# Performance work log

Hardware: AMD Instinct MI355X
Metric: run time of the kernel (lower is better)

## Reference

```python
import jax, jax.numpy as jnp
import numpy as np


def setup_inputs() -> dict:
    key = jax.random.key(0)
    kq, kk, kv = jax.random.split(key, 3)
    B, L, S, H, E = 4, 2048, 2048, 16, 64
    queries = jax.random.normal(kq, (B, L, H, E), dtype=jnp.float32)
    keys = jax.random.normal(kk, (B, S, H, E), dtype=jnp.float32)
    values = jax.random.normal(kv, (B, S, H, E), dtype=jnp.float32)
    return {"queries": queries, "keys": keys, "values": values}


def reference(queries, keys, values):
    # queries: [b,l,h,e], keys: [b,s,h,e], values: [b,s,h,d]
    e = queries.shape[-1]
    scale = 1.0 / jnp.sqrt(jnp.asarray(e, dtype=queries.dtype))
    scores = jnp.einsum('blhe,bshe->bhls', queries, keys)  # [b,h,l,s]
    attn_map = jax.nn.softmax(scale * scores, axis=-1)
    # dropout is identity in eval/reference mode
    v = jnp.einsum('bhls,bshd->blhd', attn_map, values)  # [b,l,h,d]
    return v, attn_map
```

## Files before the change

### kernel.cpp

```cpp
#include <hip/hip_runtime.h>
#include <hip/hip_bf16.h>


typedef __attribute__((ext_vector_type(4)))  float  f32x4;
typedef __attribute__((ext_vector_type(8)))  short  short8;
typedef __attribute__((ext_vector_type(4)))  short  short4v;
typedef __attribute__((ext_vector_type(4)))  unsigned short u16x4;

__device__ __forceinline__ unsigned short bf(float x) {
  return __builtin_bit_cast(unsigned short, __float2bfloat16(x));
}

__device__ __forceinline__ float bf2f(unsigned short u) {
  return __builtin_bit_cast(float, (unsigned int)u << 16);
}

__device__ __forceinline__ unsigned short f2bf(float f) {
  unsigned int u = __builtin_bit_cast(unsigned int, f);
  return (unsigned short)((u + 0x7FFFu + ((u >> 16) & 1u)) >> 16);
}

#define MFMA16(A, Bv, C) __builtin_amdgcn_mfma_f32_16x16x32_bf16(A, Bv, C, 0, 0, 0)


__global__ __launch_bounds__(256) void conv_all(const float* __restrict__ K,
                                                const float* __restrict__ V,
                                                unsigned short* __restrict__ Kbf,
                                                unsigned short* __restrict__ VTbf) {
  __shared__ unsigned short T[64][68];
  if (blockIdx.x < 4096) {
    int idx = blockIdx.x * 256 + threadIdx.x;
    int e0 = (idx & 7) << 3;
    int h  = (idx >> 3) & 15;
    int l  = (idx >> 7) & 2047;
    int b  = idx >> 18;
    const float* src = K + (((size_t)(b * 2048 + l)) * 16 + h) * 64 + e0;
    unsigned short* dst = Kbf + (((size_t)(b * 16 + h)) * 2048 + l) * 64 + e0;
    float4 a = *(const float4*)src;
    float4 c = *(const float4*)(src + 4);
    u16x4 o0 = { bf(a.x), bf(a.y), bf(a.z), bf(a.w) };
    u16x4 o1 = { bf(c.x), bf(c.y), bf(c.z), bf(c.w) };
    *(u16x4*)dst = o0;
    *(u16x4*)(dst + 4) = o1;
  } else {
    int bid = blockIdx.x - 4096;
    int sc = bid & 31, bh = bid >> 5;
    int h = bh & 15, b = bh >> 4;
    int t = threadIdx.x;
    int srow = t >> 2, d0 = (t & 3) << 4;
    const float* src = V + (((size_t)(b * 2048 + sc * 64 + srow)) * 16 + h) * 64 + d0;
    float4 v0 = *(const float4*)(src + 0);
    float4 v1 = *(const float4*)(src + 4);
    float4 v2 = *(const float4*)(src + 8);
    float4 v3 = *(const float4*)(src + 12);
    T[d0+ 0][srow]=bf(v0.x); T[d0+ 1][srow]=bf(v0.y); T[d0+ 2][srow]=bf(v0.z); T[d0+ 3][srow]=bf(v0.w);
    T[d0+ 4][srow]=bf(v1.x); T[d0+ 5][srow]=bf(v1.y); T[d0+ 6][srow]=bf(v1.z); T[d0+ 7][srow]=bf(v1.w);
    T[d0+ 8][srow]=bf(v2.x); T[d0+ 9][srow]=bf(v2.y); T[d0+10][srow]=bf(v2.z); T[d0+11][srow]=bf(v2.w);
    T[d0+12][srow]=bf(v3.x); T[d0+13][srow]=bf(v3.y); T[d0+14][srow]=bf(v3.z); T[d0+15][srow]=bf(v3.w);
    __syncthreads();
    int d = t >> 2, s0 = (t & 3) << 4;
    unsigned short* dst = VTbf + ((size_t)bh * 64 + d) * 2048 + sc * 64 + s0;
#pragma unroll
    for (int j = 0; j < 16; j += 4) {
      u16x4 x = { T[d][s0 + j], T[d][s0 + j + 1], T[d][s0 + j + 2], T[d][s0 + j + 3] };
      *(u16x4*)(dst + j) = x;
    }
  }
}


__device__ __forceinline__ void gll16(const void* g, void* l) {
  __builtin_amdgcn_global_load_lds(
      (const __attribute__((address_space(1))) unsigned int*)g,
      (__attribute__((address_space(3))) unsigned int*)l, 16, 0, 0);
}

__device__ __forceinline__ void stage8(const unsigned short* gsrc, int rowStride,
                                       unsigned short* dstRow0, int lane) {
  int rr = lane >> 3;
  int cc = ((lane & 7) ^ rr) << 3;
  gll16(gsrc + (size_t)rr * rowStride + cc, dstRow0);
}

__device__ __forceinline__ short8 frag(const unsigned short* tile, int row, int colb) {
  return *(const short8*)((const char*)tile + row * 128 + (colb ^ ((row & 7) << 4)));
}

__global__ __launch_bounds__(512, 2) void attn_main(
    const float* __restrict__ Qf, const unsigned short* __restrict__ Kbf,
    const unsigned short* __restrict__ VTbf, float* __restrict__ Og,
    float* __restrict__ Ag) {

  int wg = ((blockIdx.x & 7) << 7) | (blockIdx.x >> 3);
  int qt = wg & 15, bh = wg >> 4;
  int h = bh & 15, b = bh >> 4;

  int tid = threadIdx.x, lane = tid & 63, w = tid >> 6;
  int g = lane >> 4, r16 = lane & 15;
  int q0 = qt * 128;

  __shared__ __align__(16) unsigned short Qb[128][64];
  __shared__ __align__(16) unsigned short Kb[2][64][64];
  __shared__ __align__(16) unsigned short Vb[2][64][64];
  __shared__ __align__(16) unsigned short Pb[8][16][72];

  const unsigned short* kg = Kbf + (size_t)bh * 2048 * 64 + (size_t)(w * 8) * 64;
  const unsigned short* vg = VTbf + (size_t)bh * 64 * 2048 + (size_t)(w * 8) * 2048;

  {
    const float sc = 0.18033688011112042f;
    int row = tid >> 2, c0 = (tid & 3) << 4;
    const float* qsrc = Qf + (((size_t)(b * 2048 + q0 + row)) * 16 + h) * 64 + c0;
    float4 qa = *(const float4*)(qsrc + 0);
    float4 qb = *(const float4*)(qsrc + 4);
    float4 qc = *(const float4*)(qsrc + 8);
    float4 qd = *(const float4*)(qsrc + 12);
    stage8(kg,            64, &Kb[0][w * 8][0], lane);
    stage8(kg + 4096,     64, &Kb[1][w * 8][0], lane);
    stage8(kg + 2 * 4096, 64, &Vb[0][w * 8][0], lane);
    stage8(kg + 3 * 4096, 64, &Vb[1][w * 8][0], lane);
    unsigned short* qdst = &Qb[row][c0];
    u16x4 o0 = { bf(qa.x*sc), bf(qa.y*sc), bf(qa.z*sc), bf(qa.w*sc) };
    u16x4 o1 = { bf(qb.x*sc), bf(qb.y*sc), bf(qb.z*sc), bf(qb.w*sc) };
    u16x4 o2 = { bf(qc.x*sc), bf(qc.y*sc), bf(qc.z*sc), bf(qc.w*sc) };
    u16x4 o3 = { bf(qd.x*sc), bf(qd.y*sc), bf(qd.z*sc), bf(qd.w*sc) };
    *(u16x4*)(qdst + 0) = o0;  *(u16x4*)(qdst + 4)  = o1;
    *(u16x4*)(qdst + 8) = o2;  *(u16x4*)(qdst + 12) = o3;
  }
  asm volatile("s_waitcnt lgkmcnt(0)" ::: "memory");
  __builtin_amdgcn_s_barrier();

  short8 qf0 = *(const short8*)((const char*)&Qb[w * 16 + r16][0] + g * 16);
  short8 qf1 = *(const short8*)((const char*)&Qb[w * 16 + r16][0] + 64 + g * 16);

  float lsum = 0.0f;
  for (int ii = 0; ii < 16; ++ii) {
    const int hsel = ii & 1;
    const unsigned short* sA = hsel ? &Vb[0][0][0] : &Kb[0][0][0];
    const unsigned short* sB = hsel ? &Vb[1][0][0] : &Kb[1][0][0];

    if (ii < 15) {
      asm volatile("s_waitcnt vmcnt(2)" ::: "memory");
    } else {
      asm volatile("s_waitcnt vmcnt(0)" ::: "memory");
    }
    __builtin_amdgcn_s_barrier();

    f32x4 st[8];
    __builtin_amdgcn_s_setprio(1);
#pragma unroll
    for (int t = 0; t < 4; ++t) {
      short8 kf0 = frag(sA, t * 16 + r16, g * 16);
      short8 kf1 = frag(sA, t * 16 + r16, 64 + g * 16);
      f32x4 z = {0.f, 0.f, 0.f, 0.f};
      z = MFMA16(kf0, qf0, z);
      z = MFMA16(kf1, qf1, z);
      st[t] = z;
    }
#pragma unroll
    for (int t = 0; t < 4; ++t) {
      short8 kf0 = frag(sB, t * 16 + r16, g * 16);
      short8 kf1 = frag(sB, t * 16 + r16, 64 + g * 16);
      f32x4 z = {0.f, 0.f, 0.f, 0.f};
      z = MFMA16(kf0, qf0, z);
      z = MFMA16(kf1, qf1, z);
      st[t + 4] = z;
    }
    __builtin_amdgcn_s_setprio(0);

    float acc = 0.f;
#pragma unroll
    for (int t = 0; t < 8; ++t) {
      float e0 = __builtin_amdgcn_exp2f(st[t][0]) + __builtin_amdgcn_exp2f(st[t][1]);
      float e1 = __builtin_amdgcn_exp2f(st[t][2]) + __builtin_amdgcn_exp2f(st[t][3]);
      acc += e0 + e1;
    }
    lsum += acc;

    __builtin_amdgcn_s_barrier();

    if (ii < 14) {
      const unsigned short* nk = kg + (size_t)(2 * ii + 4) * 4096;
      unsigned short* dA = hsel ? &Vb[0][w * 8][0] : &Kb[0][w * 8][0];
      unsigned short* dB = hsel ? &Vb[1][w * 8][0] : &Kb[1][w * 8][0];
      stage8(nk,        64, dA, lane);
      stage8(nk + 4096, 64, dB, lane);
    }
  }
  lsum += __shfl_xor(lsum, 16, 64);
  lsum += __shfl_xor(lsum, 32, 64);
  float rinv = 1.0f / lsum;

  f32x4 oacc[4];
#pragma unroll
  for (int t = 0; t < 4; ++t) oacc[t] = (f32x4){0.f, 0.f, 0.f, 0.f};

  stage8(kg, 64, &Kb[0][w * 8][0], lane);
  stage8(vg, 2048, &Vb[0][w * 8][0], lane);
  asm volatile("s_waitcnt vmcnt(0)" ::: "memory");
  __builtin_amdgcn_s_barrier();
  int cur = 0;

  float* aW = Ag + ((size_t)bh * 2048 + (size_t)(q0 + w * 16)) * 2048;
  const int sra = lane >> 4;
  const int src4 = (lane & 15) * 4;

  for (int ch = 0; ch < 32; ++ch) {
    if (ch < 31) {
      stage8(kg + (size_t)(ch + 1) * 4096, 64, &Kb[cur ^ 1][w * 8][0], lane);
      stage8(vg + (size_t)(ch + 1) * 64, 2048, &Vb[cur ^ 1][w * 8][0], lane);
    }
    f32x4 st[4];
    __builtin_amdgcn_s_setprio(1);
#pragma unroll
    for (int t = 0; t < 4; ++t) {
      short8 kf0 = frag(&Kb[cur][0][0], t * 16 + r16, g * 16);
      short8 kf1 = frag(&Kb[cur][0][0], t * 16 + r16, 64 + g * 16);
      f32x4 z = {0.f, 0.f, 0.f, 0.f};
      z = MFMA16(kf0, qf0, z);
      z = MFMA16(kf1, qf1, z);
      st[t] = z;
    }
    __builtin_amdgcn_s_setprio(0);

#pragma unroll
    for (int t = 0; t < 4; ++t) {
      f32x4 p;
#pragma unroll
      for (int r = 0; r < 4; ++r)
        p[r] = __builtin_amdgcn_exp2f(st[t][r]) * rinv;
      u16x4 pb = { bf(p[0]), bf(p[1]), bf(p[2]), bf(p[3]) };
      *(u16x4*)&Pb[w][r16][t * 16 + 4 * g] = pb;
    }

#pragma unroll
    for (int i = 0; i < 4; ++i) {
      int row = 4 * i + sra;
      u16x4 pb4 = *(const u16x4*)&Pb[w][row][src4];
      f32x4 o = { bf2f(pb4[0]), bf2f(pb4[1]), bf2f(pb4[2]), bf2f(pb4[3]) };
      __builtin_nontemporal_store(o, (f32x4*)(aW + (size_t)row * 2048 + ch * 64 + src4));
    }

    __builtin_amdgcn_s_setprio(1);
#pragma unroll
    for (int c = 0; c < 2; ++c) {
      short8 pa = *(const short8*)((const char*)&Pb[w][r16][0] + c * 64 + g * 16);
#pragma unroll
      for (int t = 0; t < 4; ++t) {
        short8 vf = frag(&Vb[cur][0][0], t * 16 + r16, c * 64 + g * 16);
        oacc[t] = MFMA16(pa, vf, oacc[t]);
      }
    }
    __builtin_amdgcn_s_setprio(0);

    asm volatile("s_waitcnt vmcnt(4)" ::: "memory");
    __builtin_amdgcn_s_barrier();
    cur ^= 1;
  }

  float* op = Og + (((size_t)b * 2048 + (size_t)(q0 + w * 16 + 4 * g)) * 16 + h) * 64;
#pragma unroll
  for (int t = 0; t < 4; ++t)
#pragma unroll
    for (int r = 0; r < 4; ++r)
      op[(size_t)r * 1024 + t * 16 + r16] = oacc[t][r];
}


__global__ __launch_bounds__(256, 2) void attn_fused(
    const float* __restrict__ Qg, const float* __restrict__ Kg,
    const float* __restrict__ Vg, float* __restrict__ Og,
    float* __restrict__ Ag) {

  const int qt = blockIdx.x & 31;
  const int bh = blockIdx.x >> 5;
  const int h  = bh & 15;
  const int b  = bh >> 4;

  const int tid  = threadIdx.x;
  const int lane = tid & 63;
  const int w    = tid >> 6;
  const int g    = lane >> 4;
  const int r16  = lane & 15;

  __shared__ __align__(16) unsigned short Qbuf[64][72];
  __shared__ __align__(16) unsigned short Kbuf[64][72];
  __shared__ __align__(16) unsigned short VT[64][68];
  __shared__ __align__(16) unsigned short Pbuf[4][16][72];

  const size_t inbase = (size_t)b * (2048u * 1024u) + (size_t)h * 64u;
  const int q0 = qt << 6;

  const int srow = tid >> 2;
  const int sd0  = (tid & 3) << 4;

  {
    const float sc = 0.18033688011112042f;
    const float* gp = Qg + inbase + (size_t)(q0 + srow) * 1024u + sd0;
    float4 va = *(const float4*)(gp + 0);
    float4 vb = *(const float4*)(gp + 4);
    float4 vc = *(const float4*)(gp + 8);
    float4 vd = *(const float4*)(gp + 12);
    unsigned short* dst = &Qbuf[srow][sd0];
    dst[0]=f2bf(va.x*sc); dst[1]=f2bf(va.y*sc); dst[2]=f2bf(va.z*sc); dst[3]=f2bf(va.w*sc);
    dst[4]=f2bf(vb.x*sc); dst[5]=f2bf(vb.y*sc); dst[6]=f2bf(vb.z*sc); dst[7]=f2bf(vb.w*sc);
    dst[8]=f2bf(vc.x*sc); dst[9]=f2bf(vc.y*sc); dst[10]=f2bf(vc.z*sc); dst[11]=f2bf(vc.w*sc);
    dst[12]=f2bf(vd.x*sc); dst[13]=f2bf(vd.y*sc); dst[14]=f2bf(vd.z*sc); dst[15]=f2bf(vd.w*sc);
  }
  __syncthreads();

  const short8 qf0 = *(const short8*)&Qbuf[w*16 + r16][g*8];
  const short8 qf1 = *(const short8*)&Qbuf[w*16 + r16][32 + g*8];

  f32x4 mrow = { -3e38f, -3e38f, -3e38f, -3e38f };
  f32x4 lrow = { 0.f, 0.f, 0.f, 0.f };

  for (int ch = 0; ch < 32; ++ch) {
    __syncthreads();
    {
      const float* gp = Kg + inbase + (size_t)(ch*64 + srow) * 1024u + sd0;
      float4 va = *(const float4*)(gp + 0);
      float4 vb = *(const float4*)(gp + 4);
      float4 vc = *(const float4*)(gp + 8);
      float4 vd = *(const float4*)(gp + 12);
      unsigned short* dst = &Kbuf[srow][sd0];
      dst[0]=f2bf(va.x); dst[1]=f2bf(va.y); dst[2]=f2bf(va.z); dst[3]=f2bf(va.w);
      dst[4]=f2bf(vb.x); dst[5]=f2bf(vb.y); dst[6]=f2bf(vb.z); dst[7]=f2bf(vb.w);
      dst[8]=f2bf(vc.x); dst[9]=f2bf(vc.y); dst[10]=f2bf(vc.z); dst[11]=f2bf(vc.w);
      dst[12]=f2bf(vd.x); dst[13]=f2bf(vd.y); dst[14]=f2bf(vd.z); dst[15]=f2bf(vd.w);
    }
    __syncthreads();

    f32x4 st[4];
#pragma unroll
    for (int t = 0; t < 4; ++t) {
      const short8 kf0 = *(const short8*)&Kbuf[t*16 + r16][g*8];
      const short8 kf1 = *(const short8*)&Kbuf[t*16 + r16][32 + g*8];
      f32x4 z = {0.f, 0.f, 0.f, 0.f};
      z = MFMA16(qf0, kf0, z);
      z = MFMA16(qf1, kf1, z);
      st[t] = z;
    }

    f32x4 cm = st[0];
#pragma unroll
    for (int t = 1; t < 4; ++t)
#pragma unroll
      for (int r = 0; r < 4; ++r) cm[r] = fmaxf(cm[r], st[t][r]);
#pragma unroll
    for (int i = 1; i < 16; i <<= 1)
#pragma unroll
      for (int r = 0; r < 4; ++r) cm[r] = fmaxf(cm[r], __shfl_xor(cm[r], i, 64));

    f32x4 mn, corr, sum = {0.f, 0.f, 0.f, 0.f};
#pragma unroll
    for (int r = 0; r < 4; ++r) {
      mn[r]   = fmaxf(mrow[r], cm[r]);
      corr[r] = exp2f(mrow[r] - mn[r]);
    }
#pragma unroll
    for (int t = 0; t < 4; ++t)
#pragma unroll
      for (int r = 0; r < 4; ++r) sum[r] += exp2f(st[t][r] - mn[r]);
#pragma unroll
    for (int i = 1; i < 16; i <<= 1)
#pragma unroll
      for (int r = 0; r < 4; ++r) sum[r] += __shfl_xor(sum[r], i, 64);
#pragma unroll
    for (int r = 0; r < 4; ++r) {
      lrow[r] = lrow[r] * corr[r] + sum[r];
      mrow[r] = mn[r];
    }
  }

  f32x4 rinv;
#pragma unroll
  for (int r = 0; r < 4; ++r) rinv[r] = 1.0f / lrow[r];

  f32x4 oacc[4];
#pragma unroll
  for (int t = 0; t < 4; ++t) oacc[t] = (f32x4){0.f, 0.f, 0.f, 0.f};

  float* aRow = Ag + ((size_t)bh * 2048u + (size_t)(q0 + w*16 + 4*g)) * 2048u;

  for (int ch = 0; ch < 32; ++ch) {
    __syncthreads();
    {
      const float* gp = Kg + inbase + (size_t)(ch*64 + srow) * 1024u + sd0;
      float4 va = *(const float4*)(gp + 0);
      float4 vb = *(const float4*)(gp + 4);
      float4 vc = *(const float4*)(gp + 8);
      float4 vd = *(const float4*)(gp + 12);
      unsigned short* dst = &Kbuf[srow][sd0];
      dst[0]=f2bf(va.x); dst[1]=f2bf(va.y); dst[2]=f2bf(va.z); dst[3]=f2bf(va.w);
      dst[4]=f2bf(vb.x); dst[5]=f2bf(vb.y); dst[6]=f2bf(vb.z); dst[7]=f2bf(vb.w);
      dst[8]=f2bf(vc.x); dst[9]=f2bf(vc.y); dst[10]=f2bf(vc.z); dst[11]=f2bf(vc.w);
      dst[12]=f2bf(vd.x); dst[13]=f2bf(vd.y); dst[14]=f2bf(vd.z); dst[15]=f2bf(vd.w);
    }
    {
      const float* gp = Vg + inbase + (size_t)(ch*64 + lane) * 1024u + (size_t)(w*16);
      float4 va = *(const float4*)(gp + 0);
      float4 vb = *(const float4*)(gp + 4);
      float4 vc = *(const float4*)(gp + 8);
      float4 vd = *(const float4*)(gp + 12);
      const int dbase = w * 16;
      VT[dbase+ 0][lane]=f2bf(va.x); VT[dbase+ 1][lane]=f2bf(va.y);
      VT[dbase+ 2][lane]=f2bf(va.z); VT[dbase+ 3][lane]=f2bf(va.w);
      VT[dbase+ 4][lane]=f2bf(vb.x); VT[dbase+ 5][lane]=f2bf(vb.y);
      VT[dbase+ 6][lane]=f2bf(vb.z); VT[dbase+ 7][lane]=f2bf(vb.w);
      VT[dbase+ 8][lane]=f2bf(vc.x); VT[dbase+ 9][lane]=f2bf(vc.y);
      VT[dbase+10][lane]=f2bf(vc.z); VT[dbase+11][lane]=f2bf(vc.w);
      VT[dbase+12][lane]=f2bf(vd.x); VT[dbase+13][lane]=f2bf(vd.y);
      VT[dbase+14][lane]=f2bf(vd.z); VT[dbase+15][lane]=f2bf(vd.w);
    }
    __syncthreads();

    f32x4 st[4];
#pragma unroll
    for (int t = 0; t < 4; ++t) {
      const short8 kf0 = *(const short8*)&Kbuf[t*16 + r16][g*8];
      const short8 kf1 = *(const short8*)&Kbuf[t*16 + r16][32 + g*8];
      f32x4 z = {0.f, 0.f, 0.f, 0.f};
      z = MFMA16(qf0, kf0, z);
      z = MFMA16(qf1, kf1, z);
      st[t] = z;
    }

#pragma unroll
    for (int t = 0; t < 4; ++t) {
#pragma unroll
      for (int r = 0; r < 4; ++r) {
        float p = exp2f(st[t][r] - mrow[r]) * rinv[r];
        aRow[(size_t)r * 2048u + (size_t)(ch*64 + t*16 + r16)] = p;
        Pbuf[w][4*g + r][t*16 + r16] = f2bf(p);
      }
    }

#pragma unroll
    for (int c = 0; c < 2; ++c) {
      const short8 pa = *(const short8*)&Pbuf[w][r16][c*32 + g*8];
#pragma unroll
      for (int t = 0; t < 4; ++t) {
        const unsigned short* vp = &VT[t*16 + r16][c*32 + g*8];
        short4v lo = *(const short4v*)vp;
        short4v hi = *(const short4v*)(vp + 4);
        short8 vbf = { lo[0], lo[1], lo[2], lo[3], hi[0], hi[1], hi[2], hi[3] };
        oacc[t] = MFMA16(pa, vbf, oacc[t]);
      }
    }
  }

  float* op = Og + (((size_t)b * 2048u + (size_t)(q0 + w*16 + 4*g)) * 16u + (size_t)h) * 64u;
#pragma unroll
  for (int t = 0; t < 4; ++t)
#pragma unroll
    for (int r = 0; r < 4; ++r)
      op[(size_t)r * 1024u + (size_t)(t*16 + r16)] = oacc[t][r];
}


extern "C" void kernel_launch(void* const* d_in, const int* in_sizes, int n_in,
                              void* d_out, int out_size, void* d_ws, size_t ws_size,
                              hipStream_t stream) {
  const float* Q = (const float*)d_in[0];
  const float* K = (const float*)d_in[1];
  const float* V = (const float*)d_in[2];
  float* Og = (float*)d_out;
  float* Ag = (float*)d_out + 8388608;

  const size_t NEED = 2ull * 8388608ull * 2ull;
  if (ws_size >= NEED) {
    unsigned short* Kbf  = (unsigned short*)d_ws;
    unsigned short* VTbf = Kbf + 8388608;
    conv_all<<<dim3(6144), dim3(256), 0, stream>>>(K, V, Kbf, VTbf);
    attn_main<<<dim3(1024), dim3(512), 0, stream>>>(Q, Kbf, VTbf, Og, Ag);
  } else {
    attn_fused<<<dim3(2048), dim3(256), 0, stream>>>(Q, K, V, Og, Ag);
  }
}
```

Before: 237.5 us.

## Process two query tiles per block, fusing tile B's row-sum into tile A's pass

```diff
diff --git a/kernel.cpp b/kernel.cpp
--- a/kernel.cpp
+++ b/kernel.cpp
@@ -86,20 +86,33 @@
   return *(const short8*)((const char*)tile + row * 128 + (colb ^ ((row & 7) << 4)));
 }
 
+__device__ __forceinline__ void load_qfrag(const float* __restrict__ Qf, int b, int h,
+                                           int q, int g, short8* qf0, short8* qf1) {
+  const float sc = 0.18033688011112042f;
+  const float* p = Qf + (((size_t)(b * 2048 + q)) * 16 + h) * 64 + g * 8;
+  float4 a0 = *(const float4*)(p + 0);
+  float4 a1 = *(const float4*)(p + 4);
+  float4 b0 = *(const float4*)(p + 32);
+  float4 b1 = *(const float4*)(p + 36);
+  *qf0 = (short8){ (short)bf(a0.x*sc), (short)bf(a0.y*sc), (short)bf(a0.z*sc), (short)bf(a0.w*sc),
+                   (short)bf(a1.x*sc), (short)bf(a1.y*sc), (short)bf(a1.z*sc), (short)bf(a1.w*sc) };
+  *qf1 = (short8){ (short)bf(b0.x*sc), (short)bf(b0.y*sc), (short)bf(b0.z*sc), (short)bf(b0.w*sc),
+                   (short)bf(b1.x*sc), (short)bf(b1.y*sc), (short)bf(b1.z*sc), (short)bf(b1.w*sc) };
+}
+
 __global__ __launch_bounds__(512, 2) void attn_main(
     const float* __restrict__ Qf, const unsigned short* __restrict__ Kbf,
     const unsigned short* __restrict__ VTbf, float* __restrict__ Og,
     float* __restrict__ Ag) {
 
-  int wg = ((blockIdx.x & 7) << 7) | (blockIdx.x >> 3);
-  int qt = wg & 15, bh = wg >> 4;
+  int wg = ((blockIdx.x & 7) << 6) | (blockIdx.x >> 3);
+  int qp = wg & 7, bh = wg >> 3;
   int h = bh & 15, b = bh >> 4;
 
   int tid = threadIdx.x, lane = tid & 63, w = tid >> 6;
   int g = lane >> 4, r16 = lane & 15;
-  int q0 = qt * 128;
-
-  __shared__ __align__(16) unsigned short Qb[128][64];
+  int q0A = qp * 256, q0B = q0A + 128;
+
   __shared__ __align__(16) unsigned short Kb[2][64][64];
   __shared__ __align__(16) unsigned short Vb[2][64][64];
   __shared__ __align__(16) unsigned short Pb[8][16][72];
@@ -107,31 +120,14 @@
   const unsigned short* kg = Kbf + (size_t)bh * 2048 * 64 + (size_t)(w * 8) * 64;
   const unsigned short* vg = VTbf + (size_t)bh * 64 * 2048 + (size_t)(w * 8) * 2048;
 
-  {
-    const float sc = 0.18033688011112042f;
-    int row = tid >> 2, c0 = (tid & 3) << 4;
-    const float* qsrc = Qf + (((size_t)(b * 2048 + q0 + row)) * 16 + h) * 64 + c0;
-    float4 qa = *(const float4*)(qsrc + 0);
-    float4 qb = *(const float4*)(qsrc + 4);
-    float4 qc = *(const float4*)(qsrc + 8);
-    float4 qd = *(const float4*)(qsrc + 12);
-    stage8(kg,            64, &Kb[0][w * 8][0], lane);
-    stage8(kg + 4096,     64, &Kb[1][w * 8][0], lane);
-    stage8(kg + 2 * 4096, 64, &Vb[0][w * 8][0], lane);
-    stage8(kg + 3 * 4096, 64, &Vb[1][w * 8][0], lane);
-    unsigned short* qdst = &Qb[row][c0];
-    u16x4 o0 = { bf(qa.x*sc), bf(qa.y*sc), bf(qa.z*sc), bf(qa.w*sc) };
-    u16x4 o1 = { bf(qb.x*sc), bf(qb.y*sc), bf(qb.z*sc), bf(qb.w*sc) };
-    u16x4 o2 = { bf(qc.x*sc), bf(qc.y*sc), bf(qc.z*sc), bf(qc.w*sc) };
-    u16x4 o3 = { bf(qd.x*sc), bf(qd.y*sc), bf(qd.z*sc), bf(qd.w*sc) };
-    *(u16x4*)(qdst + 0) = o0;  *(u16x4*)(qdst + 4)  = o1;
-    *(u16x4*)(qdst + 8) = o2;  *(u16x4*)(qdst + 12) = o3;
-  }
-  asm volatile("s_waitcnt lgkmcnt(0)" ::: "memory");
-  __builtin_amdgcn_s_barrier();
-
-  short8 qf0 = *(const short8*)((const char*)&Qb[w * 16 + r16][0] + g * 16);
-  short8 qf1 = *(const short8*)((const char*)&Qb[w * 16 + r16][0] + 64 + g * 16);
+  short8 qfA0, qfA1, qfB0, qfB1;
+  load_qfrag(Qf, b, h, q0A + w * 16 + r16, g, &qfA0, &qfA1);
+  load_qfrag(Qf, b, h, q0B + w * 16 + r16, g, &qfB0, &qfB1);
+
+  stage8(kg,            64, &Kb[0][w * 8][0], lane);
+  stage8(kg + 4096,     64, &Kb[1][w * 8][0], lane);
+  stage8(kg + 2 * 4096, 64, &Vb[0][w * 8][0], lane);
+  stage8(kg + 3 * 4096, 64, &Vb[1][w * 8][0], lane);
 
   float lsum = 0.0f;
   for (int ii = 0; ii < 16; ++ii) {
@@ -153,8 +149,8 @@
       short8 kf0 = frag(sA, t * 16 + r16, g * 16);
       short8 kf1 = frag(sA, t * 16 + r16, 64 + g * 16);
       f32x4 z = {0.f, 0.f, 0.f, 0.f};
-      z = MFMA16(kf0, qf0, z);
-      z = MFMA16(kf1, qf1, z);
+      z = MFMA16(kf0, qfA0, z);
+      z = MFMA16(kf1, qfA1, z);
       st[t] = z;
     }
 #pragma unroll
@@ -162,8 +158,8 @@
       short8 kf0 = frag(sB, t * 16 + r16, g * 16);
       short8 kf1 = frag(sB, t * 16 + r16, 64 + g * 16);
       f32x4 z = {0.f, 0.f, 0.f, 0.f};
-      z = MFMA16(kf0, qf0, z);
-      z = MFMA16(kf1, qf1, z);
+      z = MFMA16(kf0, qfA0, z);
+      z = MFMA16(kf1, qfA1, z);
       st[t + 4] = z;
     }
     __builtin_amdgcn_s_setprio(0);
@@ -189,11 +185,11 @@
   }
   lsum += __shfl_xor(lsum, 16, 64);
   lsum += __shfl_xor(lsum, 32, 64);
-  float rinv = 1.0f / lsum;
-
-  f32x4 oacc[4];
-#pragma unroll
-  for (int t = 0; t < 4; ++t) oacc[t] = (f32x4){0.f, 0.f, 0.f, 0.f};
+  float rinvA = 1.0f / lsum;
+
+  f32x4 oaccA[4];
+#pragma unroll
+  for (int t = 0; t < 4; ++t) oaccA[t] = (f32x4){0.f, 0.f, 0.f, 0.f};
 
   stage8(kg, 64, &Kb[0][w * 8][0], lane);
   stage8(vg, 2048, &Vb[0][w * 8][0], lane);
@@ -201,34 +197,43 @@
   __builtin_amdgcn_s_barrier();
   int cur = 0;
 
-  float* aW = Ag + ((size_t)bh * 2048 + (size_t)(q0 + w * 16)) * 2048;
+  float* aWA = Ag + ((size_t)bh * 2048 + (size_t)(q0A + w * 16)) * 2048;
+  float* aWB = Ag + ((size_t)bh * 2048 + (size_t)(q0B + w * 16)) * 2048;
   const int sra = lane >> 4;
   const int src4 = (lane & 15) * 4;
 
+  float lsumB = 0.0f;
   for (int ch = 0; ch < 32; ++ch) {
     if (ch < 31) {
       stage8(kg + (size_t)(ch + 1) * 4096, 64, &Kb[cur ^ 1][w * 8][0], lane);
       stage8(vg + (size_t)(ch + 1) * 64, 2048, &Vb[cur ^ 1][w * 8][0], lane);
     }
     f32x4 st[4];
+    float bacc = 0.f;
     __builtin_amdgcn_s_setprio(1);
 #pragma unroll
     for (int t = 0; t < 4; ++t) {
       short8 kf0 = frag(&Kb[cur][0][0], t * 16 + r16, g * 16);
       short8 kf1 = frag(&Kb[cur][0][0], t * 16 + r16, 64 + g * 16);
-      f32x4 z = {0.f, 0.f, 0.f, 0.f};
-      z = MFMA16(kf0, qf0, z);
-      z = MFMA16(kf1, qf1, z);
-      st[t] = z;
+      f32x4 zA = {0.f, 0.f, 0.f, 0.f};
+      zA = MFMA16(kf0, qfA0, zA);
+      zA = MFMA16(kf1, qfA1, zA);
+      st[t] = zA;
+      f32x4 zB = {0.f, 0.f, 0.f, 0.f};
+      zB = MFMA16(kf0, qfB0, zB);
+      zB = MFMA16(kf1, qfB1, zB);
+      bacc += (__builtin_amdgcn_exp2f(zB[0]) + __builtin_amdgcn_exp2f(zB[1])) +
+              (__builtin_amdgcn_exp2f(zB[2]) + __builtin_amdgcn_exp2f(zB[3]));
     }
     __builtin_amdgcn_s_setprio(0);
+    lsumB += bacc;
 
 #pragma unroll
     for (int t = 0; t < 4; ++t) {
       f32x4 p;
 #pragma unroll
       for (int r = 0; r < 4; ++r)
-        p[r] = __builtin_amdgcn_exp2f(st[t][r]) * rinv;
+        p[r] = __builtin_amdgcn_exp2f(st[t][r]) * rinvA;
       u16x4 pb = { bf(p[0]), bf(p[1]), bf(p[2]), bf(p[3]) };
       *(u16x4*)&Pb[w][r16][t * 16 + 4 * g] = pb;
     }
@@ -238,7 +243,7 @@
       int row = 4 * i + sra;
       u16x4 pb4 = *(const u16x4*)&Pb[w][row][src4];
       f32x4 o = { bf2f(pb4[0]), bf2f(pb4[1]), bf2f(pb4[2]), bf2f(pb4[3]) };
-      __builtin_nontemporal_store(o, (f32x4*)(aW + (size_t)row * 2048 + ch * 64 + src4));
+      __builtin_nontemporal_store(o, (f32x4*)(aWA + (size_t)row * 2048 + ch * 64 + src4));
     }
 
     __builtin_amdgcn_s_setprio(1);
@@ -248,7 +253,7 @@
 #pragma unroll
       for (int t = 0; t < 4; ++t) {
         short8 vf = frag(&Vb[cur][0][0], t * 16 + r16, c * 64 + g * 16);
-        oacc[t] = MFMA16(pa, vf, oacc[t]);
+        oaccA[t] = MFMA16(pa, vf, oaccA[t]);
       }
     }
     __builtin_amdgcn_s_setprio(0);
@@ -258,12 +263,90 @@
     cur ^= 1;
   }
 
-  float* op = Og + (((size_t)b * 2048 + (size_t)(q0 + w * 16 + 4 * g)) * 16 + h) * 64;
-#pragma unroll
-  for (int t = 0; t < 4; ++t)
-#pragma unroll
-    for (int r = 0; r < 4; ++r)
-      op[(size_t)r * 1024 + t * 16 + r16] = oacc[t][r];
+  {
+    float* op = Og + (((size_t)b * 2048 + (size_t)(q0A + w * 16 + 4 * g)) * 16 + h) * 64;
+#pragma unroll
+    for (int t = 0; t < 4; ++t)
+#pragma unroll
+      for (int r = 0; r < 4; ++r)
+        op[(size_t)r * 1024 + t * 16 + r16] = oaccA[t][r];
+  }
+
+  lsumB += __shfl_xor(lsumB, 16, 64);
+  lsumB += __shfl_xor(lsumB, 32, 64);
+  float rinvB = 1.0f / lsumB;
+
+  f32x4 oaccB[4];
+#pragma unroll
+  for (int t = 0; t < 4; ++t) oaccB[t] = (f32x4){0.f, 0.f, 0.f, 0.f};
+
+  stage8(kg, 64, &Kb[0][w * 8][0], lane);
+  stage8(vg, 2048, &Vb[0][w * 8][0], lane);
+  asm volatile("s_waitcnt vmcnt(0)" ::: "memory");
+  __builtin_amdgcn_s_barrier();
+  cur = 0;
+
+  for (int ch = 0; ch < 32; ++ch) {
+    if (ch < 31) {
+      stage8(kg + (size_t)(ch + 1) * 4096, 64, &Kb[cur ^ 1][w * 8][0], lane);
+      stage8(vg + (size_t)(ch + 1) * 64, 2048, &Vb[cur ^ 1][w * 8][0], lane);
+    }
+    f32x4 st[4];
+    __builtin_amdgcn_s_setprio(1);
+#pragma unroll
+    for (int t = 0; t < 4; ++t) {
+      short8 kf0 = frag(&Kb[cur][0][0], t * 16 + r16, g * 16);
+      short8 kf1 = frag(&Kb[cur][0][0], t * 16 + r16, 64 + g * 16);
+      f32x4 z = {0.f, 0.f, 0.f, 0.f};
+      z = MFMA16(kf0, qfB0, z);
+      z = MFMA16(kf1, qfB1, z);
+      st[t] = z;
+    }
+    __builtin_amdgcn_s_setprio(0);
+
+#pragma unroll
+    for (int t = 0; t < 4; ++t) {
+      f32x4 p;
+#pragma unroll
+      for (int r = 0; r < 4; ++r)
+        p[r] = __builtin_amdgcn_exp2f(st[t][r]) * rinvB;
+      u16x4 pb = { bf(p[0]), bf(p[1]), bf(p[2]), bf(p[3]) };
+      *(u16x4*)&Pb[w][r16][t * 16 + 4 * g] = pb;
+    }
+
+#pragma unroll
+    for (int i = 0; i < 4; ++i) {
+      int row = 4 * i + sra;
+      u16x4 pb4 = *(const u16x4*)&Pb[w][row][src4];
+      f32x4 o = { bf2f(pb4[0]), bf2f(pb4[1]), bf2f(pb4[2]), bf2f(pb4[3]) };
+      __builtin_nontemporal_store(o, (f32x4*)(aWB + (size_t)row * 2048 + ch * 64 + src4));
+    }
+
+    __builtin_amdgcn_s_setprio(1);
+#pragma unroll
+    for (int c = 0; c < 2; ++c) {
+      short8 pa = *(const short8*)((const char*)&Pb[w][r16][0] + c * 64 + g * 16);
+#pragma unroll
+      for (int t = 0; t < 4; ++t) {
+        short8 vf = frag(&Vb[cur][0][0], t * 16 + r16, c * 64 + g * 16);
+        oaccB[t] = MFMA16(pa, vf, oaccB[t]);
+      }
+    }
+    __builtin_amdgcn_s_setprio(0);
+
+    asm volatile("s_waitcnt vmcnt(4)" ::: "memory");
+    __builtin_amdgcn_s_barrier();
+    cur ^= 1;
+  }
+
+  {
+    float* op = Og + (((size_t)b * 2048 + (size_t)(q0B + w * 16 + 4 * g)) * 16 + h) * 64;
+#pragma unroll
+    for (int t = 0; t < 4; ++t)
+#pragma unroll
+      for (int r = 0; r < 4; ++r)
+        op[(size_t)r * 1024 + t * 16 + r16] = oaccB[t][r];
+  }
 }
 
 
@@ -473,7 +556,7 @@
     unsigned short* Kbf  = (unsigned short*)d_ws;
     unsigned short* VTbf = Kbf + 8388608;
     conv_all<<<dim3(6144), dim3(256), 0, stream>>>(K, V, Kbf, VTbf);
-    attn_main<<<dim3(1024), dim3(512), 0, stream>>>(Q, Kbf, VTbf, Og, Ag);
+    attn_main<<<dim3(512), dim3(512), 0, stream>>>(Q, Kbf, VTbf, Og, Ag);
   } else {
     attn_fused<<<dim3(2048), dim3(256), 0, stream>>>(Q, K, V, Og, Ag);
   }
```

Measured after the change: 266.2 us. 1.12x slower.

## Use 32x32 MFMA with split key tiles in softmax denominator pass

Applied to the files above, without the earlier changes.

```diff
diff --git a/kernel.cpp b/kernel.cpp
--- a/kernel.cpp
+++ b/kernel.cpp
@@ -3,10 +3,13 @@
 
 
 typedef __attribute__((ext_vector_type(4)))  float  f32x4;
+typedef __attribute__((ext_vector_type(16))) float  f32x16;
 typedef __attribute__((ext_vector_type(8)))  short  short8;
 typedef __attribute__((ext_vector_type(4)))  short  short4v;
 typedef __attribute__((ext_vector_type(4)))  unsigned short u16x4;
 
+#define Z16 {0.f,0.f,0.f,0.f,0.f,0.f,0.f,0.f,0.f,0.f,0.f,0.f,0.f,0.f,0.f,0.f}
+
 __device__ __forceinline__ unsigned short bf(float x) {
   return __builtin_bit_cast(unsigned short, __float2bfloat16(x));
 }
@@ -21,6 +24,7 @@
 }
 
 #define MFMA16(A, Bv, C) __builtin_amdgcn_mfma_f32_16x16x32_bf16(A, Bv, C, 0, 0, 0)
+#define MFMA32(A, Bv, C) __builtin_amdgcn_mfma_f32_32x32x16_bf16(A, Bv, C, 0, 0, 0)
 
 
 __global__ __launch_bounds__(256) void conv_all(const float* __restrict__ K,
@@ -97,12 +101,14 @@
 
   int tid = threadIdx.x, lane = tid & 63, w = tid >> 6;
   int g = lane >> 4, r16 = lane & 15;
+  int cl = lane & 31, hi = lane >> 5;
   int q0 = qt * 128;
 
   __shared__ __align__(16) unsigned short Qb[128][64];
   __shared__ __align__(16) unsigned short Kb[2][64][64];
   __shared__ __align__(16) unsigned short Vb[2][64][64];
   __shared__ __align__(16) unsigned short Pb[8][16][72];
+  __shared__ float Ps[2][128];
 
   const unsigned short* kg = Kbf + (size_t)bh * 2048 * 64 + (size_t)(w * 8) * 64;
   const unsigned short* vg = VTbf + (size_t)bh * 64 * 2048 + (size_t)(w * 8) * 2048;
@@ -130,14 +136,18 @@
   asm volatile("s_waitcnt lgkmcnt(0)" ::: "memory");
   __builtin_amdgcn_s_barrier();
 
-  short8 qf0 = *(const short8*)((const char*)&Qb[w * 16 + r16][0] + g * 16);
-  short8 qf1 = *(const short8*)((const char*)&Qb[w * 16 + r16][0] + 64 + g * 16);
+  const int qg = w & 3, half = w >> 2;
+
+  short8 qp[4];
+#pragma unroll
+  for (int kc = 0; kc < 4; ++kc)
+    qp[kc] = *(const short8*)((const char*)&Qb[qg * 32 + cl][0] + kc * 32 + hi * 16);
 
   float lsum = 0.0f;
   for (int ii = 0; ii < 16; ++ii) {
     const int hsel = ii & 1;
-    const unsigned short* sA = hsel ? &Vb[0][0][0] : &Kb[0][0][0];
-    const unsigned short* sB = hsel ? &Vb[1][0][0] : &Kb[1][0][0];
+    const unsigned short* tA = hsel ? &Vb[0][0][0] : &Kb[0][0][0];
+    const unsigned short* tB = hsel ? &Vb[1][0][0] : &Kb[1][0][0];
 
     if (ii < 15) {
       asm volatile("s_waitcnt vmcnt(2)" ::: "memory");
@@ -146,36 +156,31 @@
     }
     __builtin_amdgcn_s_barrier();
 
-    f32x4 st[8];
+    const unsigned short* kt = half ? tB : tA;
+    f32x16 z0 = Z16, z1 = Z16;
     __builtin_amdgcn_s_setprio(1);
 #pragma unroll
-    for (int t = 0; t < 4; ++t) {
-      short8 kf0 = frag(sA, t * 16 + r16, g * 16);
-      short8 kf1 = frag(sA, t * 16 + r16, 64 + g * 16);
-      f32x4 z = {0.f, 0.f, 0.f, 0.f};
-      z = MFMA16(kf0, qf0, z);
-      z = MFMA16(kf1, qf1, z);
-      st[t] = z;
-    }
-#pragma unroll
-    for (int t = 0; t < 4; ++t) {
-      short8 kf0 = frag(sB, t * 16 + r16, g * 16);
-      short8 kf1 = frag(sB, t * 16 + r16, 64 + g * 16);
-      f32x4 z = {0.f, 0.f, 0.f, 0.f};
-      z = MFMA16(kf0, qf0, z);
-      z = MFMA16(kf1, qf1, z);
-      st[t + 4] = z;
+    for (int kc = 0; kc < 4; ++kc) {
+      short8 ka0 = frag(kt, cl,      kc * 32 + hi * 16);
+      short8 ka1 = frag(kt, 32 + cl, kc * 32 + hi * 16);
+      z0 = MFMA32(ka0, qp[kc], z0);
+      z1 = MFMA32(ka1, qp[kc], z1);
     }
     __builtin_amdgcn_s_setprio(0);
 
-    float acc = 0.f;
-#pragma unroll
-    for (int t = 0; t < 8; ++t) {
-      float e0 = __builtin_amdgcn_exp2f(st[t][0]) + __builtin_amdgcn_exp2f(st[t][1]);
-      float e1 = __builtin_amdgcn_exp2f(st[t][2]) + __builtin_amdgcn_exp2f(st[t][3]);
-      acc += e0 + e1;
-    }
-    lsum += acc;
+    float a0 = 0.f, a1 = 0.f, a2 = 0.f, a3 = 0.f;
+#pragma unroll
+    for (int r = 0; r < 4; ++r) {
+      a0 += __builtin_amdgcn_exp2f(z0[r]);
+      a1 += __builtin_amdgcn_exp2f(z0[4 + r]);
+      a2 += __builtin_amdgcn_exp2f(z0[8 + r]);
+      a3 += __builtin_amdgcn_exp2f(z0[12 + r]);
+      a0 += __builtin_amdgcn_exp2f(z1[r]);
+      a1 += __builtin_amdgcn_exp2f(z1[4 + r]);
+      a2 += __builtin_amdgcn_exp2f(z1[8 + r]);
+      a3 += __builtin_amdgcn_exp2f(z1[12 + r]);
+    }
+    lsum += (a0 + a1) + (a2 + a3);
 
     __builtin_amdgcn_s_barrier();
 
@@ -187,16 +192,22 @@
       stage8(nk + 4096, 64, dB, lane);
     }
   }
-  lsum += __shfl_xor(lsum, 16, 64);
   lsum += __shfl_xor(lsum, 32, 64);
-  float rinv = 1.0f / lsum;
+  if (lane < 32) Ps[half][qg * 32 + cl] = lsum;
 
   f32x4 oacc[4];
 #pragma unroll
   for (int t = 0; t < 4; ++t) oacc[t] = (f32x4){0.f, 0.f, 0.f, 0.f};
 
+  asm volatile("s_waitcnt lgkmcnt(0)" ::: "memory");
+  __builtin_amdgcn_s_barrier();
   stage8(kg, 64, &Kb[0][w * 8][0], lane);
   stage8(vg, 2048, &Vb[0][w * 8][0], lane);
+
+  short8 qf0 = *(const short8*)((const char*)&Qb[w * 16 + r16][0] + g * 16);
+  short8 qf1 = *(const short8*)((const char*)&Qb[w * 16 + r16][0] + 64 + g * 16);
+  float rinv = 1.0f / (Ps[0][w * 16 + r16] + Ps[1][w * 16 + r16]);
+
   asm volatile("s_waitcnt vmcnt(0)" ::: "memory");
   __builtin_amdgcn_s_barrier();
   int cur = 0;
```

Measured after the change: 238.2 us. Within noise of the previous version (+0.3%).
